# Optimization experiments

Hardware: AMD Instinct MI355X
Metric: run time of the kernel (lower is better)

Reference implementation:

```python
import jax, jax.numpy as jnp
import numpy as np

# Dims: b=2, C=256 (in_channels), IC=128 (inter_channels), H=W=64, N=4096
B, C, IC, H, W = 2, 256, 128, 64, 64
N = H * W
K_RATIO = 0.5
BN_EPS = 1e-5


def setup_inputs() -> dict:
    key = jax.random.key(0)
    ks = jax.random.split(key, 12)
    s = 0.05
    return {
        "x": jax.random.normal(ks[0], (B, C, H, W), dtype=jnp.float32),
        "hard_map": jax.random.uniform(ks[1], (B, 1, H, W), dtype=jnp.float32),
        # 1x1 conv weights stored as (out_ch, in_ch)
        "Wg": jax.random.normal(ks[2], (IC, C), dtype=jnp.float32) * s,
        "bg": jnp.zeros((IC,), dtype=jnp.float32),
        "Wth": jax.random.normal(ks[3], (IC, C), dtype=jnp.float32) * s,
        "bth": jnp.zeros((IC,), dtype=jnp.float32),
        "Wph": jax.random.normal(ks[4], (IC, C), dtype=jnp.float32) * s,
        "bph": jnp.zeros((IC,), dtype=jnp.float32),
        # GCN weight: inter -> inter
        "Wgcn": jax.random.normal(ks[5], (IC, IC), dtype=jnp.float32) * s,
        # w_gcn: 1x1 conv inter -> in_channels, then BatchNorm affine
        "Wout": jax.random.normal(ks[6], (C, IC), dtype=jnp.float32) * s,
        "bout": jnp.zeros((C,), dtype=jnp.float32),
        "gamma": jnp.ones((C,), dtype=jnp.float32),
        "beta": jnp.zeros((C,), dtype=jnp.float32),
    }


def _conv1x1(x, Wc, bc):
    # x: (b, cin, H, W), Wc: (cout, cin)
    return jnp.einsum("bchw,oc->bohw", x, Wc) + bc[None, :, None, None]


def reference(x, hard_map, Wg, bg, Wth, bth, Wph, bph, Wgcn, Wout, bout, gamma, beta):
    b, c, h, w = x.shape
    n = h * w
    ic = Wg.shape[0]

    # g/theta/phi 1x1 projections, flattened to nodes
    g_x = _conv1x1(x, Wg, bg).reshape(b, ic, n).transpose(0, 2, 1)      # (b, N, IC)
    theta_x = _conv1x1(x, Wth, bth).reshape(b, ic, n).transpose(0, 2, 1)  # (b, N, IC)
    phi_x = _conv1x1(x, Wph, bph).reshape(b, ic, n)                      # (b, IC, N)

    # Dense non-local attention, softmax over keys
    att = jax.nn.softmax(jnp.einsum("bnc,bcm->bnm", theta_x, phi_x), axis=-1)  # (b,N,N)

    # grid_2_COO (no_grad in torch): keep top-k entries per row (k = k_ratio*N),
    # restrict rows to 'hard' pixels from hard_map, row-renormalize.
    k = int(K_RATIO * n)
    kth = jax.lax.top_k(att, k)[0][..., -1:]                  # (b,N,1) k-th largest per row
    hard = (hard_map.reshape(b, n) > 0.5).astype(att.dtype)   # (b,N) hard-pixel mask
    A = jnp.where(att >= kth, att, jnp.zeros((), att.dtype)) * hard[:, :, None]
    A = A / (A.sum(axis=-1, keepdims=True) + 1e-6)
    A = jax.lax.stop_gradient(A)  # built under torch.no_grad

    # GCN: relu(A (X W))
    gc = jax.nn.relu(jnp.einsum("bnm,bmc->bnc", A, g_x @ Wgcn))  # (b,N,IC)

    # back to image layout, w_gcn 1x1 conv + BatchNorm (training-mode stats)
    gc = gc.reshape(b, h, w, ic).transpose(0, 3, 1, 2)  # (b,IC,H,W)
    y = _conv1x1(gc, Wout, bout)                        # (b,C,H,W)
    mean = y.mean(axis=(0, 2, 3))
    var = y.var(axis=(0, 2, 3))
    y = (y - mean[None, :, None, None]) * jax.lax.rsqrt(var + BN_EPS)[None, :, None, None]
    y = gamma[None, :, None, None] * y + beta[None, :, None, None]

    return x + y
```

## Files before the change

kernel.cpp:

```cpp
#include <hip/hip_runtime.h>

#define B_ 2
#define C_ 256
#define IC_ 128
#define N_ 4096
#define KSEL 2048
#define KS_PV 8

#define OFF_GC    0u
#define OFF_Y     1048576u
#define OFF_MEAN  3145728u
#define OFF_RSIG  3145984u
#define OFF_CNT   3146240u
#define OFF_LIST  3146304u
#define OFF_THB   3154496u
#define OFF_PHB   3678784u
#define OFF_GWT   4203072u
#define OFF_XTH   4727360u
#define OFF_WALL  5775936u
#define OFF_BALL  5825088u
#define OFF_S     5825472u

typedef __attribute__((ext_vector_type(8))) _Float16 f16x8;
typedef __attribute__((ext_vector_type(4))) float f32x4;

__device__ __forceinline__ unsigned short f2h(float f) {
    union { _Float16 h; unsigned short u; } cv;
    cv.h = (_Float16)f;
    return cv.u;
}
__device__ __forceinline__ float h2f(unsigned short u) {
    union { unsigned short u; _Float16 h; } cv;
    cv.u = u;
    return (float)cv.h;
}

__global__ __launch_bounds__(256) void wconv_kernel(
    const float* __restrict__ Wth, const float* __restrict__ bth,
    const float* __restrict__ Wg,  const float* __restrict__ bg,
    const float* __restrict__ Wgcn,
    const float* __restrict__ Wph, const float* __restrict__ bph,
    unsigned short* __restrict__ WallH, float* __restrict__ ball)
{
    const int o = blockIdx.x;
    const int c = threadIdx.x;
    const int oo = o & 127;
    float wv, bv;
    if (o < 128) {
        wv = Wth[oo * C_ + c];
        bv = bth[oo];
    } else if (o < 256) {
        float acc = 0.f;
        for (int i = 0; i < IC_; ++i)
            acc = fmaf(Wgcn[i * IC_ + oo], Wg[i * C_ + c], acc);
        wv = acc;
        float bacc = 0.f;
        for (int i = 0; i < IC_; ++i)
            bacc = fmaf(Wgcn[i * IC_ + oo], bg[i], bacc);
        bv = bacc;
    } else {
        wv = Wph[oo * C_ + c];
        bv = bph[oo];
    }
    WallH[o * C_ + c] = f2h(wv);
    if (c == 0) ball[o] = bv;
}

__global__ __launch_bounds__(256) void xt_kernel(
    const float* __restrict__ x, unsigned short* __restrict__ xTH)
{
    __shared__ float Xs[64][65];
    const int n0 = blockIdx.x * 64, c0 = blockIdx.y * 64, b = blockIdx.z;
    const int t = threadIdx.x;
#pragma unroll
    for (int s = 0; s < 4; ++s) {
        int e4 = t + 256 * s;
        int cc = e4 >> 4, c4 = e4 & 15;
        float4 v = *(const float4*)&x[((size_t)b * C_ + c0 + cc) * N_ + n0 + c4 * 4];
        Xs[cc][c4 * 4 + 0] = v.x; Xs[cc][c4 * 4 + 1] = v.y;
        Xs[cc][c4 * 4 + 2] = v.z; Xs[cc][c4 * 4 + 3] = v.w;
    }
    __syncthreads();
#pragma unroll
    for (int s = 0; s < 4; ++s) {
        int e = t + 256 * s;
        int nn = e >> 4, c4 = e & 15;
        ushort4 h;
        h.x = f2h(Xs[c4 * 4 + 0][nn]);
        h.y = f2h(Xs[c4 * 4 + 1][nn]);
        h.z = f2h(Xs[c4 * 4 + 2][nn]);
        h.w = f2h(Xs[c4 * 4 + 3][nn]);
        *(ushort4*)&xTH[((size_t)b * N_ + n0 + nn) * C_ + c0 + c4 * 4] = h;
    }
}

__global__ __launch_bounds__(256) void proj_kernel(
    const unsigned short* __restrict__ xTH,
    const unsigned short* __restrict__ WallH, const float* __restrict__ ball,
    unsigned short* __restrict__ thetaH, unsigned short* __restrict__ gWTH,
    unsigned short* __restrict__ phiH)
{
    __shared__ unsigned short Xt[128][72];
    __shared__ unsigned short Wt[128][72];
    const int n0 = blockIdx.x * 128;
    const int pj = blockIdx.y;
    const int b  = blockIdx.z;
    const int t = threadIdx.x, w = t >> 6, lane = t & 63;
    const int lrow = lane & 15, lk = (lane >> 4) * 8;
    const int wA = (w >> 1) * 64, wB = (w & 1) * 64;

    f32x4 acc[4][4];
#pragma unroll
    for (int u = 0; u < 4; ++u)
#pragma unroll
        for (int v = 0; v < 4; ++v) acc[u][v] = (f32x4)(0.f);

    for (int kc = 0; kc < C_; kc += 64) {
        __syncthreads();
#pragma unroll
        for (int s = 0; s < 4; ++s) {
            int e4 = t + 256 * s;
            int r = e4 >> 3, k8 = e4 & 7;
            *(float4*)&Xt[r][k8 * 8] =
                *(const float4*)&xTH[((size_t)b * N_ + n0 + r) * C_ + kc + k8 * 8];
        }
#pragma unroll
        for (int s = 0; s < 4; ++s) {
            int e4 = t + 256 * s;
            int r = e4 >> 3, k8 = e4 & 7;
            *(float4*)&Wt[r][k8 * 8] =
                *(const float4*)&WallH[(size_t)(pj * 128 + r) * C_ + kc + k8 * 8];
        }
        __syncthreads();

#pragma unroll
        for (int kstep = 0; kstep < 2; ++kstep) {
            const int kk = kstep * 32 + lk;
            f16x8 af[4], bf[4];
            if (pj != 1) {
#pragma unroll
                for (int u = 0; u < 4; ++u)
                    af[u] = *(const f16x8*)&Wt[wA + u * 16 + lrow][kk];
#pragma unroll
                for (int v = 0; v < 4; ++v)
                    bf[v] = *(const f16x8*)&Xt[wB + v * 16 + lrow][kk];
            } else {
#pragma unroll
                for (int u = 0; u < 4; ++u)
                    af[u] = *(const f16x8*)&Xt[wA + u * 16 + lrow][kk];
#pragma unroll
                for (int v = 0; v < 4; ++v)
                    bf[v] = *(const f16x8*)&Wt[wB + v * 16 + lrow][kk];
            }
#pragma unroll
            for (int u = 0; u < 4; ++u)
#pragma unroll
                for (int v = 0; v < 4; ++v)
                    acc[u][v] = __builtin_amdgcn_mfma_f32_16x16x32_f16(
                        af[u], bf[v], acc[u][v], 0, 0, 0);
        }
    }

    const int crow = (lane >> 4) * 4;
    if (pj != 1) {
        unsigned short* dst = (pj == 0) ? thetaH : phiH;
        const int bb2 = (pj == 0) ? 0 : 256;
#pragma unroll
        for (int u = 0; u < 4; ++u) {
            const int ob = wA + u * 16 + crow;
            float b0 = ball[bb2 + ob + 0], b1 = ball[bb2 + ob + 1];
            float b2 = ball[bb2 + ob + 2], b3 = ball[bb2 + ob + 3];
#pragma unroll
            for (int v = 0; v < 4; ++v) {
                const int n = n0 + wB + v * 16 + lrow;
                ushort4 h;
                h.x = f2h(acc[u][v][0] + b0);
                h.y = f2h(acc[u][v][1] + b1);
                h.z = f2h(acc[u][v][2] + b2);
                h.w = f2h(acc[u][v][3] + b3);
                *(ushort4*)&dst[((size_t)b * N_ + n) * IC_ + ob] = h;
            }
        }
    } else {
#pragma unroll
        for (int v = 0; v < 4; ++v) {
            const int o = wB + v * 16 + lrow;
            const float bo = ball[128 + o];
#pragma unroll
            for (int u = 0; u < 4; ++u) {
                const int nb = n0 + wA + u * 16 + crow;
                ushort4 h;
                h.x = f2h(acc[u][v][0] + bo);
                h.y = f2h(acc[u][v][1] + bo);
                h.z = f2h(acc[u][v][2] + bo);
                h.w = f2h(acc[u][v][3] + bo);
                *(ushort4*)&gWTH[((size_t)b * IC_ + o) * N_ + nb] = h;
            }
        }
    }
}

__global__ __launch_bounds__(1024) void compact_kernel(
    const float* __restrict__ hard_map, int* __restrict__ cnt,
    int* __restrict__ list)
{
    __shared__ int wsum[16];
    const int b = blockIdx.x;
    const int t = threadIdx.x, lane = t & 63, wid = t >> 6;
    const float* hm = hard_map + (size_t)b * N_;

    float4 v = *(const float4*)&hm[t * 4];
    int f0 = v.x > 0.5f, f1 = v.y > 0.5f, f2 = v.z > 0.5f, f3 = v.w > 0.5f;
    const int c = f0 + f1 + f2 + f3;

    int x = c;
#pragma unroll
    for (int off = 1; off < 64; off <<= 1) {
        int y = __shfl_up(x, off);
        if (lane >= off) x += y;
    }
    if (lane == 63) wsum[wid] = x;
    __syncthreads();
    int base = 0;
    for (int ww = 0; ww < wid; ++ww) base += wsum[ww];
    int pos = base + x - c;

    int* lst = list + b * N_;
    int n = t * 4;
    if (f0) lst[pos++] = n;
    if (f1) lst[pos++] = n + 1;
    if (f2) lst[pos++] = n + 2;
    if (f3) lst[pos++] = n + 3;

    if (t == 0) {
        int tot = 0;
#pragma unroll
        for (int ww = 0; ww < 16; ++ww) tot += wsum[ww];
        cnt[b] = tot;
    }
}

__global__ __launch_bounds__(256) void score_kernel(
    const unsigned short* __restrict__ thetaH,
    const unsigned short* __restrict__ phiH,
    const int* __restrict__ cnt, const int* __restrict__ list,
    unsigned short* __restrict__ SH, int r0base, int qr)
{
    __shared__ unsigned short Th[128][136];
    __shared__ unsigned short Ph[128][136];
    __shared__ int sIdx[128];

    const int b = blockIdx.z;
    const int count = cnt[b];
    const int lr0 = blockIdx.y * 128;
    if (r0base + lr0 >= count) return;
    const int m0 = blockIdx.x * 128;
    const int t = threadIdx.x;
    const int w = t >> 6, lane = t & 63;

    if (t < 128) {
        int gr = r0base + lr0 + t;
        sIdx[t] = (gr < count) ? list[b * N_ + gr] : -1;
    }
    __syncthreads();

#pragma unroll
    for (int s = 0; s < 8; ++s) {
        int e4 = t + 256 * s;
        int r = e4 >> 4, k4 = e4 & 15;
        int gr = sIdx[r];
        float4 v = make_float4(0.f, 0.f, 0.f, 0.f);
        if (gr >= 0)
            v = *(const float4*)&thetaH[((size_t)b * N_ + gr) * IC_ + k4 * 8];
        *(float4*)&Th[r][k4 * 8] = v;
    }
#pragma unroll
    for (int s = 0; s < 8; ++s) {
        int e4 = t + 256 * s;
        int r = e4 >> 4, k4 = e4 & 15;
        *(float4*)&Ph[r][k4 * 8] =
            *(const float4*)&phiH[((size_t)b * N_ + m0 + r) * IC_ + k4 * 8];
    }
    __syncthreads();

    const int wm = (w >> 1) * 64, wr = (w & 1) * 64;
    const int lrow = lane & 15, lk = (lane >> 4) * 8;

    f32x4 acc[4][4];
#pragma unroll
    for (int u = 0; u < 4; ++u)
#pragma unroll
        for (int v = 0; v < 4; ++v) acc[u][v] = (f32x4)(0.f);

#pragma unroll
    for (int ks = 0; ks < 4; ++ks) {
        const int kk = ks * 32 + lk;
        f16x8 af[4], bf[4];
#pragma unroll
        for (int u = 0; u < 4; ++u)
            af[u] = *(const f16x8*)&Ph[wm + u * 16 + lrow][kk];
#pragma unroll
        for (int v = 0; v < 4; ++v)
            bf[v] = *(const f16x8*)&Th[wr + v * 16 + lrow][kk];
#pragma unroll
        for (int u = 0; u < 4; ++u)
#pragma unroll
            for (int v = 0; v < 4; ++v)
                acc[u][v] = __builtin_amdgcn_mfma_f32_16x16x32_f16(
                    af[u], bf[v], acc[u][v], 0, 0, 0);
    }

    const int crow = (lane >> 4) * 4;
#pragma unroll
    for (int u = 0; u < 4; ++u) {
        const int mb = m0 + wm + u * 16 + crow;
#pragma unroll
        for (int v = 0; v < 4; ++v) {
            const int r = lr0 + wr + v * 16 + lrow;
            ushort4 h;
            h.x = f2h(acc[u][v][0]);
            h.y = f2h(acc[u][v][1]);
            h.z = f2h(acc[u][v][2]);
            h.w = f2h(acc[u][v][3]);
            *(ushort4*)&SH[((size_t)b * qr + r) * N_ + mb] = h;
        }
    }
}

__global__ __launch_bounds__(256) void select_kernel(
    unsigned short* __restrict__ SH, const int* __restrict__ cnt,
    int r0base, int qr)
{
    __shared__ unsigned int sHist[4][256];
    __shared__ unsigned int sWsum[4];
    __shared__ float sRed[8];
    __shared__ unsigned int sPrefix, sRemain;

    const int b = blockIdx.y;
    const int lr = blockIdx.x;
    if (r0base + lr >= cnt[b]) return;
    const int t = threadIdx.x, lane = t & 63, wid = t >> 6;

    uint4* row = (uint4*)(SH + ((size_t)b * qr + lr) * N_);
    uint4 rv[2];
    rv[0] = row[t];
    rv[1] = row[t + 256];

    float sv[16];
    unsigned int mu[16];
#pragma unroll
    for (int q = 0; q < 2; ++q) {
        const unsigned int* pu = (const unsigned int*)&rv[q];
#pragma unroll
        for (int dw = 0; dw < 4; ++dw) {
            unsigned int u = pu[dw];
            unsigned short h0 = (unsigned short)(u & 0xffffu);
            unsigned short h1 = (unsigned short)(u >> 16);
            int e = q * 8 + dw * 2;
            sv[e]     = h2f(h0);
            sv[e + 1] = h2f(h1);
            mu[e]     = (h0 & 0x8000u) ? (unsigned int)((~h0) & 0xffffu)
                                       : (unsigned int)(h0 | 0x8000u);
            mu[e + 1] = (h1 & 0x8000u) ? (unsigned int)((~h1) & 0xffffu)
                                       : (unsigned int)(h1 | 0x8000u);
        }
    }

    float m = -3.4e38f;
#pragma unroll
    for (int e = 0; e < 16; ++e) m = fmaxf(m, sv[e]);
#pragma unroll
    for (int off = 32; off > 0; off >>= 1) m = fmaxf(m, __shfl_xor(m, off));
    if (lane == 0) sRed[wid] = m;
    __syncthreads();
    m = fmaxf(fmaxf(sRed[0], sRed[1]), fmaxf(sRed[2], sRed[3]));

    unsigned int prefix = 0u;
    unsigned int remain = KSEL;
    for (int d = 1; d >= 0; --d) {
        __syncthreads();
#pragma unroll
        for (int ww = 0; ww < 4; ++ww) sHist[ww][t] = 0u;
        __syncthreads();
#pragma unroll
        for (int e = 0; e < 16; ++e) {
            if ((mu[e] >> (8 * (d + 1))) == prefix)
                atomicAdd(&sHist[wid][(mu[e] >> (8 * d)) & 255u], 1u);
        }
        __syncthreads();
        unsigned int x = sHist[0][t] + sHist[1][t] + sHist[2][t] + sHist[3][t];
        unsigned int own = x;
#pragma unroll
        for (int off = 1; off < 64; off <<= 1) {
            unsigned int y = __shfl_down(x, off);
            if (lane + off < 64) x += y;
        }
        if (lane == 0) sWsum[wid] = x;
        __syncthreads();
        for (int ww = wid + 1; ww < 4; ++ww) x += sWsum[ww];
        unsigned int nxt = x - own;
        if (x >= remain && nxt < remain) {
            sPrefix = (prefix << 8) | (unsigned int)t;
            sRemain = remain - nxt;
        }
        __syncthreads();
        prefix = sPrefix;
        remain = sRemain;
    }
    const unsigned int tu = prefix;

    float z = 0.f, ssel = 0.f;
#pragma unroll
    for (int e = 0; e < 16; ++e) {
        float ex = expf(sv[e] - m);
        z += ex;
        if (mu[e] >= tu) ssel += ex;
    }
#pragma unroll
    for (int off = 32; off > 0; off >>= 1) {
        z    += __shfl_xor(z, off);
        ssel += __shfl_xor(ssel, off);
    }
    __syncthreads();
    if (lane == 0) { sRed[wid] = z; sRed[4 + wid] = ssel; }
    __syncthreads();
    const float zt = sRed[0] + sRed[1] + sRed[2] + sRed[3];
    const float st = sRed[4] + sRed[5] + sRed[6] + sRed[7];
    const float inv = 1.f / (st + 1e-6f * zt);

#pragma unroll
    for (int q = 0; q < 2; ++q) {
        unsigned int* pu = (unsigned int*)&rv[q];
#pragma unroll
        for (int dw = 0; dw < 4; ++dw) {
            int e = q * 8 + dw * 2;
            unsigned int p0 = (mu[e] >= tu) ? (unsigned int)f2h(expf(sv[e] - m) * inv) : 0u;
            unsigned int p1 = (mu[e + 1] >= tu) ? (unsigned int)f2h(expf(sv[e + 1] - m) * inv) : 0u;
            pu[dw] = p0 | (p1 << 16);
        }
    }
    row[t]       = rv[0];
    row[t + 256] = rv[1];
}

__global__ __launch_bounds__(256) void pv_kernel(
    const unsigned short* __restrict__ SH, const unsigned short* __restrict__ gWTH,
    const int* __restrict__ cnt, float* __restrict__ gc_part,
    int r0base, int qr)
{
    __shared__ unsigned short Pt[64][72];
    __shared__ unsigned short Gt[128][72];

    const int b = blockIdx.z;
    const int count = cnt[b];
    const int lr0 = blockIdx.x * 64;
    if (r0base + lr0 >= count) return;
    const int ks = blockIdx.y;
    const int t = threadIdx.x;
    const int w = t >> 6, lane = t & 63;
    const int lrow = lane & 15, lk = (lane >> 4) * 8;
    const int wiA = (w & 1) * 64, wrB = (w >> 1) * 32;

    f32x4 acc[4][2];
#pragma unroll
    for (int u = 0; u < 4; ++u)
#pragma unroll
        for (int v = 0; v < 2; ++v) acc[u][v] = (f32x4)(0.f);

    for (int jc = ks * 512; jc < ks * 512 + 512; jc += 64) {
        __syncthreads();
#pragma unroll
        for (int s = 0; s < 2; ++s) {
            int e4 = t + 256 * s;
            int r = e4 >> 3, k8 = e4 & 7;
            *(float4*)&Pt[r][k8 * 8] =
                *(const float4*)&SH[((size_t)b * qr + lr0 + r) * N_ + jc + k8 * 8];
        }
#pragma unroll
        for (int s = 0; s < 4; ++s) {
            int e4 = t + 256 * s;
            int i = e4 >> 3, k8 = e4 & 7;
            *(float4*)&Gt[i][k8 * 8] =
                *(const float4*)&gWTH[((size_t)b * IC_ + i) * N_ + jc + k8 * 8];
        }
        __syncthreads();

#pragma unroll
        for (int kstep = 0; kstep < 2; ++kstep) {
            const int kk = kstep * 32 + lk;
            f16x8 af[4], bf[2];
#pragma unroll
            for (int u = 0; u < 4; ++u)
                af[u] = *(const f16x8*)&Gt[wiA + u * 16 + lrow][kk];
#pragma unroll
            for (int v = 0; v < 2; ++v)
                bf[v] = *(const f16x8*)&Pt[wrB + v * 16 + lrow][kk];
#pragma unroll
            for (int u = 0; u < 4; ++u)
#pragma unroll
                for (int v = 0; v < 2; ++v)
                    acc[u][v] = __builtin_amdgcn_mfma_f32_16x16x32_f16(
                        af[u], bf[v], acc[u][v], 0, 0, 0);
        }
    }

    const int crow = (lane >> 4) * 4;
#pragma unroll
    for (int u = 0; u < 4; ++u) {
        const int ib = wiA + u * 16 + crow;
#pragma unroll
        for (int v = 0; v < 2; ++v) {
            const int r = lr0 + wrB + v * 16 + lrow;
            *(float4*)&gc_part[(((size_t)b * KS_PV + ks) * qr + r) * IC_ + ib] =
                make_float4(acc[u][v][0], acc[u][v][1], acc[u][v][2], acc[u][v][3]);
        }
    }
}

__global__ __launch_bounds__(256) void scatter_kernel(
    const float* __restrict__ gc_part, const int* __restrict__ cnt,
    const int* __restrict__ list, float* __restrict__ gc,
    int r0base, int qr)
{
    const int b = blockIdx.y;
    int idx = blockIdx.x * 256 + threadIdx.x;
    int lr = idx >> 7, i = idx & 127;
    if (r0base + lr >= cnt[b]) return;
    float v = 0.f;
#pragma unroll
    for (int ks = 0; ks < KS_PV; ++ks)
        v += gc_part[(((size_t)b * KS_PV + ks) * qr + lr) * IC_ + i];
    int n = list[b * N_ + r0base + lr];
    gc[((size_t)b * N_ + n) * IC_ + i] = fmaxf(v, 0.f);
}

__global__ __launch_bounds__(256) void y_kernel(
    const float* __restrict__ gc, const float* __restrict__ Wout,
    const float* __restrict__ bout, float* __restrict__ y)
{
    __shared__ float Wt[64][33];
    __shared__ float Gt[32][68];
    const int n0 = blockIdx.x * 64;
    const int c0 = blockIdx.y * 64;
    const int b  = blockIdx.z;
    const int t = threadIdx.x;
    const int tx = t & 15, ty = t >> 4;

    float acc[4][4];
#pragma unroll
    for (int u = 0; u < 4; ++u)
#pragma unroll
        for (int v = 0; v < 4; ++v) acc[u][v] = 0.f;

    for (int kc = 0; kc < IC_; kc += 32) {
        __syncthreads();
#pragma unroll
        for (int s = 0; s < 2; ++s) {
            int e4 = t + 256 * s;
            int c = e4 >> 3, k4 = e4 & 7;
            float4 ww = *(const float4*)&Wout[(size_t)(c0 + c) * IC_ + kc + k4 * 4];
            Wt[c][k4 * 4 + 0] = ww.x; Wt[c][k4 * 4 + 1] = ww.y;
            Wt[c][k4 * 4 + 2] = ww.z; Wt[c][k4 * 4 + 3] = ww.w;
        }
#pragma unroll
        for (int s = 0; s < 2; ++s) {
            int e4 = t + 256 * s;
            int nn = e4 >> 3, k4 = e4 & 7;
            float4 g = *(const float4*)&gc[((size_t)b * N_ + n0 + nn) * IC_ + kc + k4 * 4];
            Gt[k4 * 4 + 0][nn] = g.x; Gt[k4 * 4 + 1][nn] = g.y;
            Gt[k4 * 4 + 2][nn] = g.z; Gt[k4 * 4 + 3][nn] = g.w;
        }
        __syncthreads();

#pragma unroll 4
        for (int k = 0; k < 32; ++k) {
            float a[4];
#pragma unroll
            for (int u = 0; u < 4; ++u) a[u] = Wt[ty * 4 + u][k];
            const float4 g4 = *(const float4*)&Gt[k][tx * 4];
            const float gm[4] = {g4.x, g4.y, g4.z, g4.w};
#pragma unroll
            for (int u = 0; u < 4; ++u)
#pragma unroll
                for (int v = 0; v < 4; ++v)
                    acc[u][v] = fmaf(a[u], gm[v], acc[u][v]);
        }
    }

#pragma unroll
    for (int u = 0; u < 4; ++u) {
        const int c = c0 + ty * 4 + u;
        const float bo = bout[c];
        *(float4*)&y[((size_t)b * C_ + c) * N_ + n0 + tx * 4] =
            make_float4(acc[u][0] + bo, acc[u][1] + bo,
                        acc[u][2] + bo, acc[u][3] + bo);
    }
}

__global__ __launch_bounds__(256) void bn_stats_kernel(
    const float* __restrict__ y, float* __restrict__ mean,
    float* __restrict__ rsig)
{
    __shared__ float sr[8];
    const int c = blockIdx.x, t = threadIdx.x;
    const int lane = t & 63, wid = t >> 6;
    float s = 0.f, ss = 0.f;
    for (int b = 0; b < B_; ++b) {
        const float* yr = y + ((size_t)b * C_ + c) * N_;
        for (int n = t; n < N_; n += 256) {
            float v = yr[n];
            s += v; ss = fmaf(v, v, ss);
        }
    }
#pragma unroll
    for (int off = 32; off > 0; off >>= 1) {
        s  += __shfl_xor(s, off);
        ss += __shfl_xor(ss, off);
    }
    if (lane == 0) { sr[wid] = s; sr[4 + wid] = ss; }
    __syncthreads();
    if (t == 0) {
        float st  = sr[0] + sr[1] + sr[2] + sr[3];
        float sst = sr[4] + sr[5] + sr[6] + sr[7];
        float mu  = st / (float)(B_ * N_);
        float var = sst / (float)(B_ * N_) - mu * mu;
        mean[c] = mu;
        rsig[c] = rsqrtf(var + 1e-5f);
    }
}

__global__ __launch_bounds__(256) void final_kernel(
    const float* __restrict__ x, const float* __restrict__ y,
    const float* __restrict__ mean, const float* __restrict__ rsig,
    const float* __restrict__ gamma, const float* __restrict__ beta,
    float* __restrict__ out)
{
    int idx = blockIdx.x * 256 + threadIdx.x;
    if (idx >= B_ * C_ * N_) return;
    int c = (idx >> 12) & (C_ - 1);
    out[idx] = x[idx] + fmaf(gamma[c], (y[idx] - mean[c]) * rsig[c], beta[c]);
}

extern "C" void kernel_launch(void* const* d_in, const int* in_sizes, int n_in,
                              void* d_out, int out_size, void* d_ws, size_t ws_size,
                              hipStream_t stream)
{
    const float* x     = (const float*)d_in[0];
    const float* hard  = (const float*)d_in[1];
    const float* Wg    = (const float*)d_in[2];
    const float* bg    = (const float*)d_in[3];
    const float* Wth   = (const float*)d_in[4];
    const float* bth   = (const float*)d_in[5];
    const float* Wph   = (const float*)d_in[6];
    const float* bph   = (const float*)d_in[7];
    const float* Wgcn  = (const float*)d_in[8];
    const float* Wout  = (const float*)d_in[9];
    const float* bout  = (const float*)d_in[10];
    const float* gamma = (const float*)d_in[11];
    const float* beta  = (const float*)d_in[12];
    float* out = (float*)d_out;
    float* ws  = (float*)d_ws;

    float* gc    = ws + OFF_GC;
    float* y     = ws + OFF_Y;
    float* mean  = ws + OFF_MEAN;
    float* rsig  = ws + OFF_RSIG;
    int*   cnt   = (int*)(ws + OFF_CNT);
    int*   list  = (int*)(ws + OFF_LIST);
    unsigned short* thetaH = (unsigned short*)(ws + OFF_THB);
    unsigned short* phiH   = (unsigned short*)(ws + OFF_PHB);
    unsigned short* gWTH   = (unsigned short*)(ws + OFF_GWT);
    unsigned short* xTH    = (unsigned short*)(ws + OFF_XTH);
    unsigned short* WallH  = (unsigned short*)(ws + OFF_WALL);
    float* ball  = ws + OFF_BALL;
    unsigned short* SH = (unsigned short*)(ws + OFF_S);

    const size_t wsf = ws_size / sizeof(float);
    int qr;
    float* gc_part;
    if (wsf >= OFF_S + (size_t)4096 * 6144) {
        qr = 4096; gc_part = ws + OFF_S + (size_t)4096 * 4096;
    } else if (wsf >= OFF_S + (size_t)2048 * 6144) {
        qr = 2048; gc_part = ws + OFF_S + (size_t)2048 * 4096;
    } else {
        qr = 1024; gc_part = out;
    }

    hipMemsetAsync(gc, 0, (size_t)B_ * N_ * IC_ * sizeof(float), stream);

    wconv_kernel<<<dim3(384), 256, 0, stream>>>(
        Wth, bth, Wg, bg, Wgcn, Wph, bph, WallH, ball);
    xt_kernel<<<dim3(N_ / 64, C_ / 64, B_), 256, 0, stream>>>(x, xTH);
    proj_kernel<<<dim3(N_ / 128, 3, B_), 256, 0, stream>>>(
        xTH, WallH, ball, thetaH, gWTH, phiH);
    compact_kernel<<<dim3(B_), 1024, 0, stream>>>(hard, cnt, list);

    for (int r0 = 0; r0 < N_; r0 += qr) {
        score_kernel<<<dim3(N_ / 128, qr / 128, B_), 256, 0, stream>>>(
            thetaH, phiH, cnt, list, SH, r0, qr);
        select_kernel<<<dim3(qr, B_), 256, 0, stream>>>(SH, cnt, r0, qr);
        pv_kernel<<<dim3(qr / 64, KS_PV, B_), 256, 0, stream>>>(
            SH, gWTH, cnt, gc_part, r0, qr);
        scatter_kernel<<<dim3(qr * IC_ / 256, B_), 256, 0, stream>>>(
            gc_part, cnt, list, gc, r0, qr);
    }

    y_kernel<<<dim3(N_ / 64, C_ / 64, B_), 256, 0, stream>>>(gc, Wout, bout, y);
    bn_stats_kernel<<<dim3(C_), 256, 0, stream>>>(y, mean, rsig);
    final_kernel<<<dim3(B_ * C_ * N_ / 256), 256, 0, stream>>>(
        x, y, mean, rsig, gamma, beta, out);
}
```

Measured before the change: 141.5 us.

## Fuse prep kernels, store PV partials in fp16, scatter via rank map

```diff
diff --git a/kernel.cpp b/kernel.cpp
--- a/kernel.cpp
+++ b/kernel.cpp
@@ -13,13 +13,14 @@
 #define OFF_RSIG  3145984u
 #define OFF_CNT   3146240u
 #define OFF_LIST  3146304u
-#define OFF_THB   3154496u
-#define OFF_PHB   3678784u
-#define OFF_GWT   4203072u
-#define OFF_XTH   4727360u
-#define OFF_WALL  5775936u
-#define OFF_BALL  5825088u
-#define OFF_S     5825472u
+#define OFF_RANK  3154496u
+#define OFF_THB   3162688u
+#define OFF_PHB   3686976u
+#define OFF_GWT   4211264u
+#define OFF_XTH   4735552u
+#define OFF_WALL  5784128u
+#define OFF_BALL  5833280u
+#define OFF_S     5833664u
 
 typedef __attribute__((ext_vector_type(8))) _Float16 f16x8;
 typedef __attribute__((ext_vector_type(4))) float f32x4;
@@ -35,62 +36,108 @@
     return (float)cv.h;
 }
 
-__global__ __launch_bounds__(256) void wconv_kernel(
+__global__ __launch_bounds__(256) void prep_kernel(
+    const float* __restrict__ x, unsigned short* __restrict__ xTH,
     const float* __restrict__ Wth, const float* __restrict__ bth,
     const float* __restrict__ Wg,  const float* __restrict__ bg,
     const float* __restrict__ Wgcn,
     const float* __restrict__ Wph, const float* __restrict__ bph,
-    unsigned short* __restrict__ WallH, float* __restrict__ ball)
-{
-    const int o = blockIdx.x;
-    const int c = threadIdx.x;
-    const int oo = o & 127;
-    float wv, bv;
-    if (o < 128) {
-        wv = Wth[oo * C_ + c];
-        bv = bth[oo];
-    } else if (o < 256) {
-        float acc = 0.f;
-        for (int i = 0; i < IC_; ++i)
-            acc = fmaf(Wgcn[i * IC_ + oo], Wg[i * C_ + c], acc);
-        wv = acc;
-        float bacc = 0.f;
-        for (int i = 0; i < IC_; ++i)
-            bacc = fmaf(Wgcn[i * IC_ + oo], bg[i], bacc);
-        bv = bacc;
+    unsigned short* __restrict__ WallH, float* __restrict__ ball,
+    const float* __restrict__ hard_map, int* __restrict__ cnt,
+    int* __restrict__ list, int* __restrict__ rank)
+{
+    __shared__ float Xs[64][65];
+    __shared__ int wsum[4];
+    const int bid = blockIdx.x;
+    const int t = threadIdx.x;
+
+    if (bid < 512) {
+        const int n0 = (bid & 63) * 64;
+        const int c0 = ((bid >> 6) & 3) * 64;
+        const int b  = bid >> 8;
+#pragma unroll
+        for (int s = 0; s < 4; ++s) {
+            int e4 = t + 256 * s;
+            int cc = e4 >> 4, c4 = e4 & 15;
+            float4 v = *(const float4*)&x[((size_t)b * C_ + c0 + cc) * N_ + n0 + c4 * 4];
+            Xs[cc][c4 * 4 + 0] = v.x; Xs[cc][c4 * 4 + 1] = v.y;
+            Xs[cc][c4 * 4 + 2] = v.z; Xs[cc][c4 * 4 + 3] = v.w;
+        }
+        __syncthreads();
+#pragma unroll
+        for (int s = 0; s < 4; ++s) {
+            int e = t + 256 * s;
+            int nn = e >> 4, c4 = e & 15;
+            ushort4 h;
+            h.x = f2h(Xs[c4 * 4 + 0][nn]);
+            h.y = f2h(Xs[c4 * 4 + 1][nn]);
+            h.z = f2h(Xs[c4 * 4 + 2][nn]);
+            h.w = f2h(Xs[c4 * 4 + 3][nn]);
+            *(ushort4*)&xTH[((size_t)b * N_ + n0 + nn) * C_ + c0 + c4 * 4] = h;
+        }
+    } else if (bid < 896) {
+        const int o = bid - 512;
+        const int c = t;
+        const int oo = o & 127;
+        float wv, bv;
+        if (o < 128) {
+            wv = Wth[oo * C_ + c];
+            bv = bth[oo];
+        } else if (o < 256) {
+            float acc = 0.f;
+            for (int i = 0; i < IC_; ++i)
+                acc = fmaf(Wgcn[i * IC_ + oo], Wg[i * C_ + c], acc);
+            wv = acc;
+            float bacc = 0.f;
+            for (int i = 0; i < IC_; ++i)
+                bacc = fmaf(Wgcn[i * IC_ + oo], bg[i], bacc);
+            bv = bacc;
+        } else {
+            wv = Wph[oo * C_ + c];
+            bv = bph[oo];
+        }
+        WallH[o * C_ + c] = f2h(wv);
+        if (c == 0) ball[o] = bv;
     } else {
-        wv = Wph[oo * C_ + c];
-        bv = bph[oo];
-    }
-    WallH[o * C_ + c] = f2h(wv);
-    if (c == 0) ball[o] = bv;
-}
-
-__global__ __launch_bounds__(256) void xt_kernel(
-    const float* __restrict__ x, unsigned short* __restrict__ xTH)
-{
-    __shared__ float Xs[64][65];
-    const int n0 = blockIdx.x * 64, c0 = blockIdx.y * 64, b = blockIdx.z;
-    const int t = threadIdx.x;
-#pragma unroll
-    for (int s = 0; s < 4; ++s) {
-        int e4 = t + 256 * s;
-        int cc = e4 >> 4, c4 = e4 & 15;
-        float4 v = *(const float4*)&x[((size_t)b * C_ + c0 + cc) * N_ + n0 + c4 * 4];
-        Xs[cc][c4 * 4 + 0] = v.x; Xs[cc][c4 * 4 + 1] = v.y;
-        Xs[cc][c4 * 4 + 2] = v.z; Xs[cc][c4 * 4 + 3] = v.w;
-    }
-    __syncthreads();
-#pragma unroll
-    for (int s = 0; s < 4; ++s) {
-        int e = t + 256 * s;
-        int nn = e >> 4, c4 = e & 15;
-        ushort4 h;
-        h.x = f2h(Xs[c4 * 4 + 0][nn]);
-        h.y = f2h(Xs[c4 * 4 + 1][nn]);
-        h.z = f2h(Xs[c4 * 4 + 2][nn]);
-        h.w = f2h(Xs[c4 * 4 + 3][nn]);
-        *(ushort4*)&xTH[((size_t)b * N_ + n0 + nn) * C_ + c0 + c4 * 4] = h;
+        const int b = bid - 896;
+        const int lane = t & 63, wid = t >> 6;
+        const float* hm = hard_map + (size_t)b * N_;
+        int flags[16];
+        int c = 0;
+#pragma unroll
+        for (int q = 0; q < 4; ++q) {
+            float4 v = *(const float4*)&hm[t * 16 + q * 4];
+            flags[q * 4 + 0] = v.x > 0.5f;
+            flags[q * 4 + 1] = v.y > 0.5f;
+            flags[q * 4 + 2] = v.z > 0.5f;
+            flags[q * 4 + 3] = v.w > 0.5f;
+            c += flags[q * 4] + flags[q * 4 + 1] + flags[q * 4 + 2] + flags[q * 4 + 3];
+        }
+        int xv = c;
+#pragma unroll
+        for (int off = 1; off < 64; off <<= 1) {
+            int y = __shfl_up(xv, off);
+            if (lane >= off) xv += y;
+        }
+        if (lane == 63) wsum[wid] = xv;
+        __syncthreads();
+        int base = 0;
+        for (int ww = 0; ww < wid; ++ww) base += wsum[ww];
+        int pos = base + xv - c;
+        int* lst = list + b * N_;
+        int* rnk = rank + b * N_;
+#pragma unroll
+        for (int e = 0; e < 16; ++e) {
+            int n = t * 16 + e;
+            if (flags[e]) { lst[pos] = n; rnk[n] = pos; ++pos; }
+            else rnk[n] = -1;
+        }
+        if (t == 0) {
+            int tot = 0;
+#pragma unroll
+            for (int ww = 0; ww < 4; ++ww) tot += wsum[ww];
+            cnt[b] = tot;
+        }
     }
 }
 
@@ -197,46 +244,6 @@
                 *(ushort4*)&gWTH[((size_t)b * IC_ + o) * N_ + nb] = h;
             }
         }
-    }
-}
-
-__global__ __launch_bounds__(1024) void compact_kernel(
-    const float* __restrict__ hard_map, int* __restrict__ cnt,
-    int* __restrict__ list)
-{
-    __shared__ int wsum[16];
-    const int b = blockIdx.x;
-    const int t = threadIdx.x, lane = t & 63, wid = t >> 6;
-    const float* hm = hard_map + (size_t)b * N_;
-
-    float4 v = *(const float4*)&hm[t * 4];
-    int f0 = v.x > 0.5f, f1 = v.y > 0.5f, f2 = v.z > 0.5f, f3 = v.w > 0.5f;
-    const int c = f0 + f1 + f2 + f3;
-
-    int x = c;
-#pragma unroll
-    for (int off = 1; off < 64; off <<= 1) {
-        int y = __shfl_up(x, off);
-        if (lane >= off) x += y;
-    }
-    if (lane == 63) wsum[wid] = x;
-    __syncthreads();
-    int base = 0;
-    for (int ww = 0; ww < wid; ++ww) base += wsum[ww];
-    int pos = base + x - c;
-
-    int* lst = list + b * N_;
-    int n = t * 4;
-    if (f0) lst[pos++] = n;
-    if (f1) lst[pos++] = n + 1;
-    if (f2) lst[pos++] = n + 2;
-    if (f3) lst[pos++] = n + 3;
-
-    if (t == 0) {
-        int tot = 0;
-#pragma unroll
-        for (int ww = 0; ww < 16; ++ww) tot += wsum[ww];
-        cnt[b] = tot;
     }
 }
 
@@ -445,7 +452,7 @@
 
 __global__ __launch_bounds__(256) void pv_kernel(
     const unsigned short* __restrict__ SH, const unsigned short* __restrict__ gWTH,
-    const int* __restrict__ cnt, float* __restrict__ gc_part,
+    const int* __restrict__ cnt, unsigned short* __restrict__ gc_partH,
     int r0base, int qr)
 {
     __shared__ unsigned short Pt[64][72];
@@ -511,26 +518,34 @@
 #pragma unroll
         for (int v = 0; v < 2; ++v) {
             const int r = lr0 + wrB + v * 16 + lrow;
-            *(float4*)&gc_part[(((size_t)b * KS_PV + ks) * qr + r) * IC_ + ib] =
-                make_float4(acc[u][v][0], acc[u][v][1], acc[u][v][2], acc[u][v][3]);
+            ushort4 h;
+            h.x = f2h(acc[u][v][0]);
+            h.y = f2h(acc[u][v][1]);
+            h.z = f2h(acc[u][v][2]);
+            h.w = f2h(acc[u][v][3]);
+            *(ushort4*)&gc_partH[(((size_t)b * KS_PV + ks) * qr + r) * IC_ + ib] = h;
         }
     }
 }
 
 __global__ __launch_bounds__(256) void scatter_kernel(
-    const float* __restrict__ gc_part, const int* __restrict__ cnt,
-    const int* __restrict__ list, float* __restrict__ gc,
-    int r0base, int qr)
+    const unsigned short* __restrict__ gc_partH, const int* __restrict__ rank,
+    float* __restrict__ gc, int r0base, int qr)
 {
     const int b = blockIdx.y;
     int idx = blockIdx.x * 256 + threadIdx.x;
-    int lr = idx >> 7, i = idx & 127;
-    if (r0base + lr >= cnt[b]) return;
+    int n = idx >> 7, i = idx & 127;
+    int r = rank[b * N_ + n];
+    if (r < 0) {
+        if (r0base == 0) gc[((size_t)b * N_ + n) * IC_ + i] = 0.f;
+        return;
+    }
+    if (r < r0base || r >= r0base + qr) return;
+    const int lr = r - r0base;
     float v = 0.f;
 #pragma unroll
     for (int ks = 0; ks < KS_PV; ++ks)
-        v += gc_part[(((size_t)b * KS_PV + ks) * qr + lr) * IC_ + i];
-    int n = list[b * N_ + r0base + lr];
+        v += h2f(gc_partH[(((size_t)b * KS_PV + ks) * qr + lr) * IC_ + i]);
     gc[((size_t)b * N_ + n) * IC_ + i] = fmaxf(v, 0.f);
 }
 
@@ -667,6 +682,7 @@
     float* rsig  = ws + OFF_RSIG;
     int*   cnt   = (int*)(ws + OFF_CNT);
     int*   list  = (int*)(ws + OFF_LIST);
+    int*   rank  = (int*)(ws + OFF_RANK);
     unsigned short* thetaH = (unsigned short*)(ws + OFF_THB);
     unsigned short* phiH   = (unsigned short*)(ws + OFF_PHB);
     unsigned short* gWTH   = (unsigned short*)(ws + OFF_GWT);
@@ -677,32 +693,29 @@
 
     const size_t wsf = ws_size / sizeof(float);
     int qr;
-    float* gc_part;
+    unsigned short* gc_partH;
     if (wsf >= OFF_S + (size_t)4096 * 6144) {
-        qr = 4096; gc_part = ws + OFF_S + (size_t)4096 * 4096;
+        qr = 4096; gc_partH = (unsigned short*)(ws + OFF_S + (size_t)4096 * 4096);
     } else if (wsf >= OFF_S + (size_t)2048 * 6144) {
-        qr = 2048; gc_part = ws + OFF_S + (size_t)2048 * 4096;
+        qr = 2048; gc_partH = (unsigned short*)(ws + OFF_S + (size_t)2048 * 4096);
     } else {
-        qr = 1024; gc_part = out;
-    }
-
-    hipMemsetAsync(gc, 0, (size_t)B_ * N_ * IC_ * sizeof(float), stream);
-
-    wconv_kernel<<<dim3(384), 256, 0, stream>>>(
-        Wth, bth, Wg, bg, Wgcn, Wph, bph, WallH, ball);
-    xt_kernel<<<dim3(N_ / 64, C_ / 64, B_), 256, 0, stream>>>(x, xTH);
+        qr = 1024; gc_partH = (unsigned short*)out;
+    }
+
+    prep_kernel<<<dim3(898), 256, 0, stream>>>(
+        x, xTH, Wth, bth, Wg, bg, Wgcn, Wph, bph, WallH, ball,
+        hard, cnt, list, rank);
     proj_kernel<<<dim3(N_ / 128, 3, B_), 256, 0, stream>>>(
         xTH, WallH, ball, thetaH, gWTH, phiH);
-    compact_kernel<<<dim3(B_), 1024, 0, stream>>>(hard, cnt, list);
 
     for (int r0 = 0; r0 < N_; r0 += qr) {
         score_kernel<<<dim3(N_ / 128, qr / 128, B_), 256, 0, stream>>>(
             thetaH, phiH, cnt, list, SH, r0, qr);
         select_kernel<<<dim3(qr, B_), 256, 0, stream>>>(SH, cnt, r0, qr);
         pv_kernel<<<dim3(qr / 64, KS_PV, B_), 256, 0, stream>>>(
-            SH, gWTH, cnt, gc_part, r0, qr);
-        scatter_kernel<<<dim3(qr * IC_ / 256, B_), 256, 0, stream>>>(
-            gc_part, cnt, list, gc, r0, qr);
+            SH, gWTH, cnt, gc_partH, r0, qr);
+        scatter_kernel<<<dim3(N_ * IC_ / 256, B_), 256, 0, stream>>>(
+            gc_partH, rank, gc, r0, qr);
     }
 
     y_kernel<<<dim3(N_ / 64, C_ / 64, B_), 256, 0, stream>>>(gc, Wout, bout, y);
```

Result: faster. 129.1 us (median of 2 runs) (-8.7%).
